# Kernel tuning notes

Hardware: AMD Instinct MI355X
Metric: run time of the kernel (lower is better)

The kernel has to match this reference:

```python
import jax, jax.numpy as jnp
import numpy as np

B, S, D, H, DH, F, K = 2, 1024, 512, 8, 64, 3072, 64

def setup_inputs() -> dict:
    key = jax.random.key(0)
    ks = jax.random.split(key, 20)
    f32 = jnp.float32
    inp = {}
    inp['resid_pre'] = jax.random.normal(ks[0], (B, S, D), f32)
    # LayerNorm scale is positive; keep it away from zero
    inp['ln_scale'] = jax.random.uniform(ks[1], (B, S, 1), f32, minval=0.5, maxval=1.5)
    # causal, row-normalized attention pattern
    p = jax.random.uniform(ks[2], (B, H, S, S), f32)
    p = jnp.tril(p) + 1e-6 * jnp.tril(jnp.ones((S, S), f32))
    inp['probs'] = p / p.sum(-1, keepdims=True)
    W_O = jax.random.normal(ks[3], (H, DH, D), f32) * 0.02
    W_V = jax.random.normal(ks[4], (H, D, DH), f32) * 0.02
    # W_OV = einsum('n_heads d_head d_out, n_heads d_model d_head -> n_heads d_model d_out')
    inp['W_OV'] = jnp.einsum('hvo,hiv->hio', W_O, W_V)
    inp['b_O'] = jax.random.normal(ks[5], (D,), f32) * 0.02
    inp['enc_w'] = jax.random.normal(ks[6], (F, D), f32) * 0.02   # downstream encoder [F, D]
    inp['enc_b'] = jax.random.normal(ks[7], (F,), f32) * 0.02
    inp['b_dec'] = jax.random.normal(ks[8], (D,), f32) * 0.02     # downstream b_dec
    inp['dec_w'] = jax.random.normal(ks[9], (D, F), f32) * 0.02   # downstream decoder [D, F]
    inp['up1_dec'] = jax.random.normal(ks[10], (D, F), f32) * 0.02
    inp['up1_bdec'] = jax.random.normal(ks[11], (D,), f32) * 0.02
    inp['pf1'] = jax.nn.relu(jax.random.normal(ks[12], (B, S, F), f32))  # pruned (TopK) features are nonneg
    inp['mask1'] = (jax.random.uniform(ks[13], (F, F)) < 0.1).astype(f32)
    inp['up2_dec'] = jax.random.normal(ks[14], (D, F), f32) * 0.02
    inp['up2_bdec'] = jax.random.normal(ks[15], (D,), f32) * 0.02
    inp['pf2'] = jax.nn.relu(jax.random.normal(ks[16], (B, S, F), f32))
    inp['mask2'] = (jax.random.uniform(ks[17], (F, F)) < 0.1).astype(f32)
    inp['feature_buffer'] = jnp.zeros((B, S, F), f32)
    inp['k'] = K
    return inp

def reference(resid_pre, ln_scale, probs, W_OV, b_O, enc_w, enc_b, b_dec, dec_w,
              up1_dec, up1_bdec, pf1, mask1, up2_dec, up2_bdec, pf2, mask2,
              feature_buffer, k):
    # ---- initial contributions (SCAEAttention.get_initial_contribs) ----
    act = resid_pre / ln_scale                                   # [b,s,i]
    pre = jnp.einsum('bsi,hio,do->bshd', act, W_OV, enc_w)       # [b,k,h,d_feat]
    approx = jnp.einsum('bhqk,bkhd->bqd', probs, pre)            # [b,q,d_feat]

    # ---- upstream pruned contributions ----
    upstream_bias = None
    for up_dec, up_bdec, pf, mask in ((up1_dec, up1_bdec, pf1, mask1),
                                      (up2_dec, up2_bdec, pf2, mask2)):
        upstream_bias = up_bdec if upstream_bias is None else upstream_bias + up_bdec
        vw = jnp.einsum('do,hio,iu->hdu', enc_w, W_OV, up_dec)   # virtual weights [h,d,u]
        vw = vw * mask[None]                                     # connection mask broadcast over heads
        up_post = pf / ln_scale                                  # [b,k,u]
        post_ov = jnp.einsum('bku,hdu->bhkd', up_post, vw)       # [b,h,k,d]
        approx = approx + jnp.einsum('bhqk,bhkd->bqd', probs, post_ov)

    # ---- bias terms (compute_bias) ----
    approx = approx + b_O @ enc_w.T + enc_b - enc_w @ b_dec
    ub = upstream_bias[None, None, :] / ln_scale                 # [b,s,i]
    ub = jnp.einsum('hio,bsi->bso', W_OV, ub)
    approx = approx + jnp.einsum('di,bsi->bsd', enc_w, ub)

    # ---- topk + relu + scatter + decode ----
    top_vals, top_idx = jax.lax.top_k(approx, k)                 # [b,s,k]
    top_vals = jax.nn.relu(top_vals)
    Bn, Sn, _ = feature_buffer.shape
    bi = jnp.arange(Bn)[:, None, None]
    si = jnp.arange(Sn)[None, :, None]
    feat_buffer = jnp.zeros_like(feature_buffer).at[bi, si, top_idx].set(top_vals)
    recon = jnp.einsum('bsf,df->bsd', feat_buffer, dec_w) + b_dec
    return (feat_buffer, recon)
```

## Files before the change

kernel.cpp:

```cpp
#include <hip/hip_runtime.h>

constexpr int B = 2, S = 1024, D = 512, H = 8, F = 3072, TOPK = 64;

typedef unsigned short u16;
typedef unsigned int u32;
typedef __attribute__((ext_vector_type(8))) short bfrag;
typedef __attribute__((ext_vector_type(4))) float f32x4;

__device__ __forceinline__ u16 f2bf_rn(float x) {
  u32 u = __float_as_uint(x);
  u32 r = (u + 0x7FFFu + ((u >> 16) & 1u)) >> 16;
  return (u16)r;
}
__device__ __forceinline__ float bf2f(u16 h) {
  return __uint_as_float(((u32)h) << 16);
}

#define GLOAD_LDS16(gp, lp)                                                   \
  __builtin_amdgcn_global_load_lds(                                           \
      (const __attribute__((address_space(1))) u32*)(gp),                     \
      (__attribute__((address_space(3))) u32*)(lp), 16, 0, 0)

__device__ __forceinline__ void stage_tile2(const u16* __restrict__ g, int r0,
                                            int ld, int k0, u16* lds,
                                            int w, int lane) {
#pragma unroll
  for (int p = 0; p < 2; ++p) {
    const int slot = w * 128 + p * 64 + lane;
    const int row = slot >> 2, sl = slot & 3;
    const int gr = sl ^ ((row >> 1) & 3);
    const u16* gp = g + (long)(r0 + row) * ld + k0 + gr * 8;
    u16* lp = lds + (w * 128 + p * 64) * 8;
    GLOAD_LDS16(gp, lp);
  }
}

__device__ __forceinline__ bfrag frag_at(const u16* tile, int row, int lg) {
  const int idx = row * 32 + ((lg ^ ((row >> 1) & 3)) << 3);
  return *(const bfrag*)(tile + idx);
}

template<bool ACCUM, bool CAUSAL, bool MASK, bool OUTPAIR>
__global__ __launch_bounds__(256) void gemm_split3(
    const u16* __restrict__ Ah0, const u16* __restrict__ Al0,
    const u16* __restrict__ Bh0, const u16* __restrict__ Bl0,
    float* __restrict__ C, u16* __restrict__ Ch, u16* __restrict__ Cl,
    const float* __restrict__ mask0, const float* __restrict__ mask1, int ldm,
    int K, int lda, int ldb, int ldc, int gx, int gy, int NB,
    long sAb, long sAh, long sBb, long sBh, long sCb, long sCh)
{
  __shared__ u16 smem[32768];

  const int nwg = gridDim.x;
  const int q = nwg >> 3, r = nwg & 7;
  const int xcd = blockIdx.x & 7, lid = blockIdx.x >> 3;
  const int sw = (xcd < r ? xcd * (q + 1) : r * (q + 1) + (xcd - r) * q) + lid;
  const int gxy = gx * gy;
  const int z = sw / gxy;
  const int rem = sw - z * gxy;
  const int by = rem / gx;
  const int bx = rem - by * gx;
  const int zb = z % NB, zh = z / NB;

  const u16* Ahp = Ah0 + zb * sAb + zh * sAh;
  const u16* Alp = Al0 + zb * sAb + zh * sAh;
  const u16* Bhp = Bh0 + zb * sBb + zh * sBh;
  const u16* Blp = Bl0 + zb * sBb + zh * sBh;
  const long coff = zb * sCb + zh * sCh;

  const int bm = by * 128, bn = bx * 128;
  const int tid = threadIdx.x;
  const int lane = tid & 63, w = tid >> 6;
  const int wr = w >> 1, wc = w & 1;
  const int lg = lane >> 4, lr = lane & 15;

  f32x4 acc[4][4];
#pragma unroll
  for (int i = 0; i < 4; ++i)
#pragma unroll
    for (int j = 0; j < 4; ++j) {
      acc[i][j][0] = 0.f; acc[i][j][1] = 0.f;
      acc[i][j][2] = 0.f; acc[i][j][3] = 0.f;
    }

  const int kmax = CAUSAL ? min(K, bm + 128) : K;
  const int nt = kmax >> 5;

#define STAGE(buf, k0)                                        \
  do {                                                        \
    u16* base_ = smem + (buf) * 16384;                        \
    stage_tile2(Ahp, bm, lda, (k0), base_,         w, lane);  \
    stage_tile2(Alp, bm, lda, (k0), base_ + 4096,  w, lane);  \
    stage_tile2(Bhp, bn, ldb, (k0), base_ + 8192,  w, lane);  \
    stage_tile2(Blp, bn, ldb, (k0), base_ + 12288, w, lane);  \
  } while (0)

  STAGE(0, 0);
  for (int t = 0; t < nt; ++t) {
    const int cur = t & 1;
    __syncthreads();
    if (t + 1 < nt) STAGE(cur ^ 1, (t + 1) << 5);
    const u16* bufp = smem + cur * 16384;
    bfrag ah[4], al4[4], bh4[4], bl4[4];
#pragma unroll
    for (int i = 0; i < 4; ++i) {
      const int rowA = wr * 64 + i * 16 + lr;
      const int rowB = wc * 64 + i * 16 + lr;
      ah[i]  = frag_at(bufp,          rowA, lg);
      al4[i] = frag_at(bufp + 4096,   rowA, lg);
      bh4[i] = frag_at(bufp + 8192,   rowB, lg);
      bl4[i] = frag_at(bufp + 12288,  rowB, lg);
    }
#pragma unroll
    for (int i = 0; i < 4; ++i)
#pragma unroll
      for (int j = 0; j < 4; ++j) {
        acc[i][j] = __builtin_amdgcn_mfma_f32_16x16x32_bf16(ah[i],  bh4[j], acc[i][j], 0, 0, 0);
        acc[i][j] = __builtin_amdgcn_mfma_f32_16x16x32_bf16(ah[i],  bl4[j], acc[i][j], 0, 0, 0);
        acc[i][j] = __builtin_amdgcn_mfma_f32_16x16x32_bf16(al4[i], bh4[j], acc[i][j], 0, 0, 0);
      }
  }
#undef STAGE

  const float* mp_ = MASK ? (zh ? mask1 : mask0) : nullptr;
#pragma unroll
  for (int i = 0; i < 4; ++i)
#pragma unroll
    for (int j = 0; j < 4; ++j)
#pragma unroll
      for (int rr = 0; rr < 4; ++rr) {
        const int row = bm + wr * 64 + i * 16 + lg * 4 + rr;
        const int col = bn + wc * 64 + j * 16 + lr;
        float v = acc[i][j][rr];
        if (MASK) v *= mp_[(long)row * ldm + col];
        const long ci = coff + (long)row * ldc + col;
        if (OUTPAIR) {
          const u16 h = f2bf_rn(v);
          Ch[ci] = h;
          Cl[ci] = f2bf_rn(v - bf2f(h));
        } else if (ACCUM) {
          C[ci] += v;
        } else {
          C[ci] = v;
        }
      }
}

__global__ void split_pair(const float* __restrict__ in, u16* __restrict__ oh,
                           u16* __restrict__ ol, long n) {
  for (long i = blockIdx.x * (long)blockDim.x + threadIdx.x; i < n;
       i += gridDim.x * (long)blockDim.x) {
    const float x = in[i];
    const u16 h = f2bf_rn(x);
    oh[i] = h;
    ol[i] = f2bf_rn(x - bf2f(h));
  }
}

__global__ void split_pair_probs(const float* __restrict__ probs, int h,
                                 u16* __restrict__ oh, u16* __restrict__ ol) {
  const long n = (long)B << 20;
  for (long i = blockIdx.x * (long)blockDim.x + threadIdx.x; i < n;
       i += gridDim.x * (long)blockDim.x) {
    const long b = i >> 20;
    const long rr = i & ((1L << 20) - 1);
    const float x = probs[(b * H + h) * (1L << 20) + rr];
    const u16 hh = f2bf_rn(x);
    oh[i] = hh;
    ol[i] = f2bf_rn(x - bf2f(hh));
  }
}

__global__ __launch_bounds__(256) void transpose_split(
    const float* __restrict__ in, const float* __restrict__ divv,
    u16* __restrict__ oh, u16* __restrict__ ol, int R, int C) {
  __shared__ float t[32][33];
  const int bx = blockIdx.x * 32;
  const int by = blockIdx.y * 32;
  const int x = threadIdx.x & 31, y = threadIdx.x >> 5;
#pragma unroll
  for (int j = 0; j < 4; ++j) {
    const int rr = by + y + j * 8;
    float v = in[(long)rr * C + bx + x];
    if (divv) v /= divv[rr];
    t[y + j * 8][x] = v;
  }
  __syncthreads();
#pragma unroll
  for (int j = 0; j < 4; ++j) {
    const int c = bx + y + j * 8;
    const float v = t[x][y + j * 8];
    const u16 h = f2bf_rn(v);
    oh[(long)c * R + by + x] = h;
    ol[(long)c * R + by + x] = f2bf_rn(v - bf2f(h));
  }
}

__global__ void cvec_partial(const float* __restrict__ W_OV,
                             const float* __restrict__ ub1,
                             const float* __restrict__ ub2,
                             float* __restrict__ ctmp) {
  const int o = blockIdx.x * 256 + threadIdx.x;
  const int h = blockIdx.y;
  const float* W = W_OV + (long)h * D * D;
  float acc = 0.f;
  for (int i = 0; i < D; ++i)
    acc = fmaf(W[(long)i * D + o], ub1[i] + ub2[i], acc);
  ctmp[h * D + o] = acc;
}

__global__ void cvec_reduce(const float* __restrict__ ctmp, float* __restrict__ cvec) {
  const int o = blockIdx.x * blockDim.x + threadIdx.x;
  if (o < D) {
    float a = 0.f;
    for (int h = 0; h < H; ++h) a += ctmp[h * D + o];
    cvec[o] = a;
  }
}

__global__ __launch_bounds__(64) void bias_vec(
    const float* __restrict__ enc_w, const float* __restrict__ b_O,
    const float* __restrict__ b_dec, const float* __restrict__ enc_b,
    const float* __restrict__ cvec, float* __restrict__ bias0,
    float* __restrict__ evec) {
  const int f = blockIdx.x;
  const int l = threadIdx.x;
  float s1 = 0.f, s2 = 0.f;
  for (int o = l; o < D; o += 64) {
    const float w = enc_w[(long)f * D + o];
    s1 = fmaf(w, b_O[o] - b_dec[o], s1);
    s2 = fmaf(w, cvec[o], s2);
  }
  for (int off = 32; off > 0; off >>= 1) {
    s1 += __shfl_down(s1, off);
    s2 += __shfl_down(s2, off);
  }
  if (l == 0) { bias0[f] = s1 + enc_b[f]; evec[f] = s2; }
}

__global__ __launch_bounds__(256) void transpose_dw(const float* __restrict__ in,
                                                    float* __restrict__ out) {
  __shared__ float t[32][33];
  const int bx = blockIdx.x * 32;
  const int by = blockIdx.y * 32;
  const int x = threadIdx.x & 31, y = threadIdx.x >> 5;
#pragma unroll
  for (int j = 0; j < 4; ++j) {
    const int row = y + j * 8;
    t[row][x] = in[(long)(by + row) * F + bx + x];
  }
  __syncthreads();
#pragma unroll
  for (int j = 0; j < 4; ++j) {
    const int row = y + j * 8;
    out[(long)(bx + row) * D + by + x] = t[x][row];
  }
}

__global__ __launch_bounds__(256) void topk_fused(
    float* __restrict__ featP, const float* __restrict__ bias0,
    const float* __restrict__ evec, const float* __restrict__ ln,
    float* __restrict__ topv, int* __restrict__ topi) {
  const int row = blockIdx.x;
  const float rln = 1.f / ln[row];
  float* p0 = featP + (long)row * F;
  __shared__ float vals[F];
  __shared__ float rv[256];
  __shared__ int ri[256];
  for (int j = threadIdx.x; j < F; j += 256)
    vals[j] = bias0[j] + evec[j] * rln + p0[j];
  __syncthreads();
  for (int j = threadIdx.x; j < F; j += 256) p0[j] = 0.f;
  __syncthreads();
  for (int it = 0; it < TOPK; ++it) {
    float best = -3.4e38f;
    int bi = F;
    for (int j = threadIdx.x; j < F; j += 256) {
      const float v = vals[j];
      if (v > best) { best = v; bi = j; }
    }
    rv[threadIdx.x] = best; ri[threadIdx.x] = bi;
    __syncthreads();
    for (int s2 = 128; s2 > 0; s2 >>= 1) {
      if (threadIdx.x < s2) {
        const float ov = rv[threadIdx.x + s2];
        const int oi = ri[threadIdx.x + s2];
        if (ov > rv[threadIdx.x] ||
            (ov == rv[threadIdx.x] && oi < ri[threadIdx.x])) {
          rv[threadIdx.x] = ov; ri[threadIdx.x] = oi;
        }
      }
      __syncthreads();
    }
    if (threadIdx.x == 0) {
      const int idx = ri[0];
      const float v = fmaxf(rv[0], 0.f);
      p0[idx] = v;
      topv[row * TOPK + it] = v;
      topi[row * TOPK + it] = idx;
      vals[idx] = -3.4e38f;
    }
    __syncthreads();
  }
}

__global__ __launch_bounds__(256) void recon_kernel(
    const float* __restrict__ topv, const int* __restrict__ topi,
    const float* __restrict__ dec_wT, const float* __restrict__ b_dec,
    float* __restrict__ recon) {
  const int row = blockIdx.x;
  __shared__ float sv[TOPK];
  __shared__ int si[TOPK];
  if (threadIdx.x < TOPK) {
    sv[threadIdx.x] = topv[row * TOPK + threadIdx.x];
    si[threadIdx.x] = topi[row * TOPK + threadIdx.x];
  }
  __syncthreads();
  const int d0 = threadIdx.x, d1 = threadIdx.x + 256;
  float a0 = b_dec[d0], a1 = b_dec[d1];
  for (int j = 0; j < TOPK; ++j) {
    const float v = sv[j];
    const float* wp = dec_wT + (long)si[j] * D;
    a0 = fmaf(v, wp[d0], a0);
    a1 = fmaf(v, wp[d1], a1);
  }
  recon[(long)row * D + d0] = a0;
  recon[(long)row * D + d1] = a1;
}

extern "C" void kernel_launch(void* const* d_in, const int* in_sizes, int n_in,
                              void* d_out, int out_size, void* d_ws, size_t ws_size,
                              hipStream_t stream) {
  const float* resid = (const float*)d_in[0];
  const float* ln    = (const float*)d_in[1];
  const float* probs = (const float*)d_in[2];
  const float* W_OV  = (const float*)d_in[3];
  const float* b_O   = (const float*)d_in[4];
  const float* enc_w = (const float*)d_in[5];
  const float* enc_b = (const float*)d_in[6];
  const float* b_dec = (const float*)d_in[7];
  const float* dec_w = (const float*)d_in[8];
  const float* up_dec_[2]  = {(const float*)d_in[9], (const float*)d_in[13]};
  const float* up_bdec_[2] = {(const float*)d_in[10], (const float*)d_in[14]};
  const float* pf_[2]      = {(const float*)d_in[11], (const float*)d_in[15]};
  const float* mask_[2]    = {(const float*)d_in[12], (const float*)d_in[16]};

  float* out_feat  = (float*)d_out;
  float* out_recon = out_feat + (size_t)B * S * F;
  float* P = out_feat;

  constexpr int NALL = D + 2 * F;
  float* ws = (float*)d_ws;
  size_t o = 0;
  float* bias0 = ws + o; o += F;
  float* evec  = ws + o; o += F;
  float* cvec  = ws + o; o += D;
  float* ctmp  = ws + o; o += (size_t)H * D;
  float* topv  = ws + o; o += (size_t)B * S * TOPK;
  int*   topi  = (int*)(ws + o); o += (size_t)B * S * TOPK;
  u16* encwPh = (u16*)(ws + o); o += (size_t)F * D / 2;
  u16* encwPl = (u16*)(ws + o); o += (size_t)F * D / 2;
  u16* wovPh  = (u16*)(ws + o); o += (size_t)H * D * D / 2;
  u16* wovPl  = (u16*)(ws + o); o += (size_t)H * D * D / 2;
  u16* udTh   = (u16*)(ws + o); o += (size_t)2 * F * D / 2;
  u16* udTl   = (u16*)(ws + o); o += (size_t)2 * F * D / 2;
  u16* Gallh  = (u16*)(ws + o); o += (size_t)B * NALL * S / 2;
  u16* Galll  = (u16*)(ws + o); o += (size_t)B * NALL * S / 2;
  u16* Phh    = (u16*)(ws + o); o += (size_t)B * S * S / 2;
  u16* Phl    = (u16*)(ws + o); o += (size_t)B * S * S / 2;
  u16* Ehh    = (u16*)(ws + o); o += (size_t)F * 512 / 2;
  u16* Ehl    = (u16*)(ws + o); o += (size_t)F * 512 / 2;
  const size_t xoff = o;
  u16* Xallh  = (u16*)(ws + o); o += (size_t)B * S * NALL / 2;
  u16* Xalll  = (u16*)(ws + o); o += (size_t)B * S * NALL / 2;
  u16* vwh    = (u16*)(ws + o); o += (size_t)F * 3072 / 2;
  u16* vwl    = (u16*)(ws + o); o += (size_t)F * 3072 / 2;
  float* dec_wT = ws + xoff;

  hipMemsetAsync(P, 0, sizeof(float) * (size_t)B * S * F, stream);

  split_pair<<<1024, 256, 0, stream>>>(enc_w, encwPh, encwPl, (long)F * D);
  split_pair<<<1024, 256, 0, stream>>>(W_OV, wovPh, wovPl, (long)H * D * D);
  for (int b = 0; b < B; ++b) {
    transpose_split<<<dim3(D / 32, S / 32), 256, 0, stream>>>(
        resid + (size_t)b * S * D, ln + (size_t)b * S,
        Gallh + ((size_t)b * NALL + 0) * S, Galll + ((size_t)b * NALL + 0) * S,
        S, D);
    for (int u = 0; u < 2; ++u)
      transpose_split<<<dim3(F / 32, S / 32), 256, 0, stream>>>(
          pf_[u] + (size_t)b * S * F, ln + (size_t)b * S,
          Gallh + ((size_t)b * NALL + 512 + (size_t)u * F) * S,
          Galll + ((size_t)b * NALL + 512 + (size_t)u * F) * S, S, F);
  }
  for (int u = 0; u < 2; ++u)
    transpose_split<<<dim3(F / 32, D / 32), 256, 0, stream>>>(
        up_dec_[u], nullptr, udTh + (size_t)u * F * D, udTl + (size_t)u * F * D,
        D, F);
  cvec_partial<<<dim3(2, 8), 256, 0, stream>>>(W_OV, up_bdec_[0], up_bdec_[1], ctmp);
  cvec_reduce<<<2, 256, 0, stream>>>(ctmp, cvec);
  bias_vec<<<F, 64, 0, stream>>>(enc_w, b_O, b_dec, enc_b, cvec, bias0, evec);

  for (int h = 0; h < H; ++h) {
    split_pair_probs<<<2048, 256, 0, stream>>>(probs, h, Phh, Phl);
    gemm_split3<false, false, false, true><<<96, 256, 0, stream>>>(
        encwPh, encwPl, wovPh + (size_t)h * D * D, wovPl + (size_t)h * D * D,
        nullptr, Ehh, Ehl, nullptr, nullptr, 0,
        512, 512, 512, 512, 4, 24, 1, 0L, 0L, 0L, 0L, 0L, 0L);
    gemm_split3<false, true, false, true><<<832, 256, 0, stream>>>(
        Phh, Phl, Gallh, Galll, nullptr, Xallh, Xalll, nullptr, nullptr, 0,
        S, S, S, NALL, NALL / 128, 8, 2,
        (long)S * S, 0L, (long)NALL * S, 0L, (long)S * NALL, 0L);
    gemm_split3<true, false, false, false><<<384, 256, 0, stream>>>(
        Xallh, Xalll, Ehh, Ehl, P, nullptr, nullptr, nullptr, nullptr, 0,
        512, NALL, 512, F, 24, 8, 2,
        (long)S * NALL, 0L, 0L, 0L, (long)S * F, 0L);

    for (int u = 0; u < 2; ++u) {
      gemm_split3<false, false, true, true><<<576, 256, 0, stream>>>(
          Ehh, Ehl, udTh + (size_t)u * F * D, udTl + (size_t)u * F * D,
          nullptr, vwh, vwl, mask_[u], nullptr, F,
          512, 512, 512, 3072, 24, 24, 1, 0L, 0L, 0L, 0L, 0L, 0L);
      gemm_split3<true, false, false, false><<<384, 256, 0, stream>>>(
          Xallh + 512 + (size_t)u * F, Xalll + 512 + (size_t)u * F,
          vwh, vwl, P, nullptr, nullptr, nullptr, nullptr, 0,
          3072, NALL, 3072, F, 24, 8, 2,
          (long)S * NALL, 0L, 0L, 0L, (long)S * F, 0L);
    }
  }

  transpose_dw<<<dim3(F / 32, D / 32), 256, 0, stream>>>(dec_w, dec_wT);
  topk_fused<<<B * S, 256, 0, stream>>>(P, bias0, evec, ln, topv, topi);
  recon_kernel<<<B * S, 256, 0, stream>>>(topv, topi, dec_wT, b_dec, out_recon);
}
```

Measured before the change: 4.426 ms.

## Use 2-wave 128x128 GEMM tiles and merge E and vw projections into one GEMM

The GEMM kernel now runs 128 threads (2 waves) per 128x128 tile. Each wave computes 128x64 with 8x4 accumulators and loads its B fragments once, reusing them across 8 A row-fragments. The host side packs the E and virtual-weight matrices side by side into one B0 buffer of width D+F, so the per-head E-projection and first upstream vw accumulation become a single GEMM with K=D+F. This cuts one kernel launch per head and one pass over P, at the cost of higher register pressure and lower per-block parallelism.

New measurement: 4.741 ms. 1.07x slower.

```diff
diff --git a/kernel.cpp b/kernel.cpp
--- a/kernel.cpp
+++ b/kernel.cpp
@@ -25,12 +25,12 @@
                                             int ld, int k0, u16* lds,
                                             int w, int lane) {
 #pragma unroll
-  for (int p = 0; p < 2; ++p) {
-    const int slot = w * 128 + p * 64 + lane;
+  for (int p = 0; p < 4; ++p) {
+    const int slot = p * 128 + w * 64 + lane;
     const int row = slot >> 2, sl = slot & 3;
     const int gr = sl ^ ((row >> 1) & 3);
     const u16* gp = g + (long)(r0 + row) * ld + k0 + gr * 8;
-    u16* lp = lds + (w * 128 + p * 64) * 8;
+    u16* lp = lds + (p * 128 + w * 64) * 8;
     GLOAD_LDS16(gp, lp);
   }
 }
@@ -41,7 +41,7 @@
 }
 
 template<bool ACCUM, bool CAUSAL, bool MASK, bool OUTPAIR>
-__global__ __launch_bounds__(256) void gemm_split3(
+__global__ __launch_bounds__(128) void gemm_split3(
     const u16* __restrict__ Ah0, const u16* __restrict__ Al0,
     const u16* __restrict__ Bh0, const u16* __restrict__ Bl0,
     float* __restrict__ C, u16* __restrict__ Ch, u16* __restrict__ Cl,
@@ -71,12 +71,11 @@
   const int bm = by * 128, bn = bx * 128;
   const int tid = threadIdx.x;
   const int lane = tid & 63, w = tid >> 6;
-  const int wr = w >> 1, wc = w & 1;
   const int lg = lane >> 4, lr = lane & 15;
 
-  f32x4 acc[4][4];
-#pragma unroll
-  for (int i = 0; i < 4; ++i)
+  f32x4 acc[8][4];
+#pragma unroll
+  for (int i = 0; i < 8; ++i)
 #pragma unroll
     for (int j = 0; j < 4; ++j) {
       acc[i][j][0] = 0.f; acc[i][j][1] = 0.f;
@@ -101,36 +100,37 @@
     __syncthreads();
     if (t + 1 < nt) STAGE(cur ^ 1, (t + 1) << 5);
     const u16* bufp = smem + cur * 16384;
-    bfrag ah[4], al4[4], bh4[4], bl4[4];
-#pragma unroll
-    for (int i = 0; i < 4; ++i) {
-      const int rowA = wr * 64 + i * 16 + lr;
-      const int rowB = wc * 64 + i * 16 + lr;
-      ah[i]  = frag_at(bufp,          rowA, lg);
-      al4[i] = frag_at(bufp + 4096,   rowA, lg);
-      bh4[i] = frag_at(bufp + 8192,   rowB, lg);
-      bl4[i] = frag_at(bufp + 12288,  rowB, lg);
-    }
-#pragma unroll
-    for (int i = 0; i < 4; ++i)
+    bfrag bh4[4], bl4[4];
+#pragma unroll
+    for (int j = 0; j < 4; ++j) {
+      const int rowB = w * 64 + j * 16 + lr;
+      bh4[j] = frag_at(bufp + 8192,  rowB, lg);
+      bl4[j] = frag_at(bufp + 12288, rowB, lg);
+    }
+#pragma unroll
+    for (int i = 0; i < 8; ++i) {
+      const int rowA = i * 16 + lr;
+      const bfrag ah = frag_at(bufp,        rowA, lg);
+      const bfrag al = frag_at(bufp + 4096, rowA, lg);
 #pragma unroll
       for (int j = 0; j < 4; ++j) {
-        acc[i][j] = __builtin_amdgcn_mfma_f32_16x16x32_bf16(ah[i],  bh4[j], acc[i][j], 0, 0, 0);
-        acc[i][j] = __builtin_amdgcn_mfma_f32_16x16x32_bf16(ah[i],  bl4[j], acc[i][j], 0, 0, 0);
-        acc[i][j] = __builtin_amdgcn_mfma_f32_16x16x32_bf16(al4[i], bh4[j], acc[i][j], 0, 0, 0);
+        acc[i][j] = __builtin_amdgcn_mfma_f32_16x16x32_bf16(ah, bh4[j], acc[i][j], 0, 0, 0);
+        acc[i][j] = __builtin_amdgcn_mfma_f32_16x16x32_bf16(ah, bl4[j], acc[i][j], 0, 0, 0);
+        acc[i][j] = __builtin_amdgcn_mfma_f32_16x16x32_bf16(al, bh4[j], acc[i][j], 0, 0, 0);
       }
+    }
   }
 #undef STAGE
 
   const float* mp_ = MASK ? (zh ? mask1 : mask0) : nullptr;
 #pragma unroll
-  for (int i = 0; i < 4; ++i)
+  for (int i = 0; i < 8; ++i)
 #pragma unroll
     for (int j = 0; j < 4; ++j)
 #pragma unroll
       for (int rr = 0; rr < 4; ++rr) {
-        const int row = bm + wr * 64 + i * 16 + lg * 4 + rr;
-        const int col = bn + wc * 64 + j * 16 + lr;
+        const int row = bm + i * 16 + lg * 4 + rr;
+        const int col = bn + w * 64 + j * 16 + lr;
         float v = acc[i][j][rr];
         if (MASK) v *= mp_[(long)row * ldm + col];
         const long ci = coff + (long)row * ldc + col;
@@ -350,6 +350,7 @@
   float* P = out_feat;
 
   constexpr int NALL = D + 2 * F;
+  constexpr int NB0  = D + F;
   float* ws = (float*)d_ws;
   size_t o = 0;
   float* bias0 = ws + o; o += F;
@@ -368,13 +369,11 @@
   u16* Galll  = (u16*)(ws + o); o += (size_t)B * NALL * S / 2;
   u16* Phh    = (u16*)(ws + o); o += (size_t)B * S * S / 2;
   u16* Phl    = (u16*)(ws + o); o += (size_t)B * S * S / 2;
-  u16* Ehh    = (u16*)(ws + o); o += (size_t)F * 512 / 2;
-  u16* Ehl    = (u16*)(ws + o); o += (size_t)F * 512 / 2;
+  u16* B0h    = (u16*)(ws + o); o += (size_t)F * NB0 / 2;
+  u16* B0l    = (u16*)(ws + o); o += (size_t)F * NB0 / 2;
   const size_t xoff = o;
   u16* Xallh  = (u16*)(ws + o); o += (size_t)B * S * NALL / 2;
   u16* Xalll  = (u16*)(ws + o); o += (size_t)B * S * NALL / 2;
-  u16* vwh    = (u16*)(ws + o); o += (size_t)F * 3072 / 2;
-  u16* vwl    = (u16*)(ws + o); o += (size_t)F * 3072 / 2;
   float* dec_wT = ws + xoff;
 
   hipMemsetAsync(P, 0, sizeof(float) * (size_t)B * S * F, stream);
@@ -402,29 +401,32 @@
 
   for (int h = 0; h < H; ++h) {
     split_pair_probs<<<2048, 256, 0, stream>>>(probs, h, Phh, Phl);
-    gemm_split3<false, false, false, true><<<96, 256, 0, stream>>>(
+    gemm_split3<false, false, false, true><<<96, 128, 0, stream>>>(
         encwPh, encwPl, wovPh + (size_t)h * D * D, wovPl + (size_t)h * D * D,
-        nullptr, Ehh, Ehl, nullptr, nullptr, 0,
-        512, 512, 512, 512, 4, 24, 1, 0L, 0L, 0L, 0L, 0L, 0L);
-    gemm_split3<false, true, false, true><<<832, 256, 0, stream>>>(
+        nullptr, B0h, B0l, nullptr, nullptr, 0,
+        512, 512, 512, NB0, 4, 24, 1, 0L, 0L, 0L, 0L, 0L, 0L);
+    gemm_split3<false, true, false, true><<<832, 128, 0, stream>>>(
         Phh, Phl, Gallh, Galll, nullptr, Xallh, Xalll, nullptr, nullptr, 0,
         S, S, S, NALL, NALL / 128, 8, 2,
         (long)S * S, 0L, (long)NALL * S, 0L, (long)S * NALL, 0L);
-    gemm_split3<true, false, false, false><<<384, 256, 0, stream>>>(
-        Xallh, Xalll, Ehh, Ehl, P, nullptr, nullptr, nullptr, nullptr, 0,
-        512, NALL, 512, F, 24, 8, 2,
-        (long)S * NALL, 0L, 0L, 0L, (long)S * F, 0L);
 
     for (int u = 0; u < 2; ++u) {
-      gemm_split3<false, false, true, true><<<576, 256, 0, stream>>>(
-          Ehh, Ehl, udTh + (size_t)u * F * D, udTl + (size_t)u * F * D,
-          nullptr, vwh, vwl, mask_[u], nullptr, F,
-          512, 512, 512, 3072, 24, 24, 1, 0L, 0L, 0L, 0L, 0L, 0L);
-      gemm_split3<true, false, false, false><<<384, 256, 0, stream>>>(
-          Xallh + 512 + (size_t)u * F, Xalll + 512 + (size_t)u * F,
-          vwh, vwl, P, nullptr, nullptr, nullptr, nullptr, 0,
-          3072, NALL, 3072, F, 24, 8, 2,
-          (long)S * NALL, 0L, 0L, 0L, (long)S * F, 0L);
+      gemm_split3<false, false, true, true><<<576, 128, 0, stream>>>(
+          B0h, B0l, udTh + (size_t)u * F * D, udTl + (size_t)u * F * D,
+          nullptr, B0h + 512, B0l + 512, mask_[u], nullptr, F,
+          512, NB0, D, NB0, 24, 24, 1, 0L, 0L, 0L, 0L, 0L, 0L);
+      if (u == 0) {
+        gemm_split3<true, false, false, false><<<384, 128, 0, stream>>>(
+            Xallh, Xalll, B0h, B0l, P, nullptr, nullptr, nullptr, nullptr, 0,
+            NB0, NALL, NB0, F, 24, 8, 2,
+            (long)S * NALL, 0L, 0L, 0L, (long)S * F, 0L);
+      } else {
+        gemm_split3<true, false, false, false><<<384, 128, 0, stream>>>(
+            Xallh + NB0, Xalll + NB0, B0h + 512, B0l + 512,
+            P, nullptr, nullptr, nullptr, nullptr, 0,
+            3072, NALL, NB0, F, 24, 8, 2,
+            (long)S * NALL, 0L, 0L, 0L, (long)S * F, 0L);
+      }
     }
   }
 
```
